# Performance work log

Measured on AMD Instinct MI355X. Metric: run time of the kernel, lower is better.

Reference implementation:

```python
import jax, jax.numpy as jnp
import numpy as np
from jax import lax

B, N, C = 16, 16384, 256          # batch, points, seed feature dim
P, NS = 256, 16                   # num_proposal, ball-query nsample
RADIUS = 0.3
NUM_CLASS, NUM_HEADING_BIN, NUM_SIZE = 18, 12, 18
OUT_FEAT = 2 + 3 + NUM_HEADING_BIN * 2 + NUM_SIZE * 4 + NUM_CLASS   # 119
PN2_NC = 128
MID_FEAT = (PN2_NC + OUT_FEAT) // 2                                 # 123
EPS = 1e-5

PARAM_NAMES = [f"mlp_{s}{i}" for i in range(3) for s in ("w", "b", "g", "be")] + [
    "c1_w", "c1_b", "bn1_g", "bn1_b", "c2_w", "c2_b", "bn2_g", "bn2_b", "c3_w", "c3_b"]


def setup_inputs():
    key = jax.random.key(0)
    ks = iter(jax.random.split(key, 32))
    def w(shape):
        return jax.random.normal(next(ks), shape, jnp.float32) / np.float32(np.sqrt(shape[0]))
    inp = {
        "pos":      jax.random.normal(next(ks), (B, N, 3), jnp.float32),
        "features": jax.random.normal(next(ks), (B, C, N), jnp.float32),
        "seed_pos": jax.random.normal(next(ks), (B, N, 3), jnp.float32),
    }
    dims = [3 + C, PN2_NC, PN2_NC, PN2_NC]
    for i in range(3):
        inp[f"mlp_w{i}"]  = w((dims[i], dims[i + 1]))
        inp[f"mlp_b{i}"]  = jnp.zeros((dims[i + 1],), jnp.float32)
        inp[f"mlp_g{i}"]  = jnp.ones((dims[i + 1],), jnp.float32)
        inp[f"mlp_be{i}"] = jnp.zeros((dims[i + 1],), jnp.float32)
    inp["c1_w"], inp["c1_b"] = w((PN2_NC, PN2_NC)), jnp.zeros((PN2_NC,), jnp.float32)
    inp["bn1_g"], inp["bn1_b"] = jnp.ones((PN2_NC,), jnp.float32), jnp.zeros((PN2_NC,), jnp.float32)
    inp["c2_w"], inp["c2_b"] = w((PN2_NC, MID_FEAT)), jnp.zeros((MID_FEAT,), jnp.float32)
    inp["bn2_g"], inp["bn2_b"] = jnp.ones((MID_FEAT,), jnp.float32), jnp.zeros((MID_FEAT,), jnp.float32)
    inp["c3_w"], inp["c3_b"] = w((MID_FEAT, OUT_FEAT)), jnp.zeros((OUT_FEAT,), jnp.float32)
    return inp


def _fps(p):
    # iterative furthest point sampling on one cloud p:[N,3] -> [P] int32 (starts at index 0)
    def step(carry, _):
        dists, far = carry
        d = jnp.sum((p - p[far]) ** 2, axis=-1)
        dists = jnp.minimum(dists, d)
        return (dists, jnp.argmax(dists).astype(jnp.int32)), far
    init = (jnp.full((p.shape[0],), 1e10, p.dtype), jnp.array(0, jnp.int32))
    _, idx = lax.scan(step, init, None, length=P)
    return idx


def _ball_query(new_pos, pos):
    # first NS points of pos within RADIUS of each center (CUDA ball_query semantics)
    d2 = jnp.sum((new_pos[:, :, None, :] - pos[:, None, :, :]) ** 2, -1)  # [B,P,N]
    n = pos.shape[1]
    ar = jnp.arange(n, dtype=jnp.int32)
    sortkey = jnp.where(d2 <= RADIUS ** 2, ar, ar + n)
    vals, idx = lax.top_k(-sortkey, NS)        # smallest keys = earliest in-radius indices
    valid = (-vals) < n
    return jnp.where(valid, idx, idx[..., :1])  # pad misses with first hit


def _bn(x, g, b, axes):
    m = jnp.mean(x, axes, keepdims=True)
    v = jnp.var(x, axes, keepdims=True)
    return (x - m) * lax.rsqrt(v + EPS) * g + b


def _forward(pos, features, seed_pos, params):
    idx_p = jax.vmap(_fps)(seed_pos)                              # seed_fps sampling [B,P]
    take = jax.vmap(lambda a, i: a[i])
    new_pos = take(pos, idx_p)                                    # [B,P,3]
    idx = _ball_query(new_pos, pos)                               # [B,P,NS]
    gp = take(pos, idx.reshape(B, -1)).reshape(B, P, NS, 3)
    gf = take(features.transpose(0, 2, 1), idx.reshape(B, -1)).reshape(B, P, NS, C)
    x = jnp.concatenate([gp - new_pos[:, :, None, :], gf], -1)    # [B,P,NS,3+C]
    for i in range(3):                                            # shared MLP (1x1 conv2d + BN + ReLU)
        x = jax.nn.relu(_bn(x @ params[f"mlp_w{i}"] + params[f"mlp_b{i}"],
                            params[f"mlp_g{i}"], params[f"mlp_be{i}"], (0, 1, 2)))
    x = jnp.max(x, axis=2)                                        # max over neighbors -> [B,P,128]
    x = jax.nn.relu(_bn(x @ params["c1_w"] + params["c1_b"], params["bn1_g"], params["bn1_b"], (0, 1)))
    x = jax.nn.relu(_bn(x @ params["c2_w"] + params["c2_b"], params["bn2_g"], params["bn2_b"], (0, 1)))
    x = x @ params["c3_w"] + params["c3_b"]                       # [B,P,OUT_FEAT]
    return x.transpose(0, 2, 1)                                   # [B,OUT_FEAT,P] like torch Conv1d


def reference(pos, features, seed_pos, mlp_w0, mlp_b0, mlp_g0, mlp_be0, mlp_w1, mlp_b1, mlp_g1, mlp_be1, mlp_w2, mlp_b2, mlp_g2, mlp_be2, c1_w, c1_b, bn1_g, bn1_b, c2_w, c2_b, bn2_g, bn2_b, c3_w, c3_b):
    ps = [mlp_w0, mlp_b0, mlp_g0, mlp_be0, mlp_w1, mlp_b1, mlp_g1, mlp_be1,
          mlp_w2, mlp_b2, mlp_g2, mlp_be2, c1_w, c1_b, bn1_g, bn1_b,
          c2_w, c2_b, bn2_g, bn2_b, c3_w, c3_b]
    params = dict(zip(PARAM_NAMES, ps))
    return _forward(pos, features, seed_pos, params)
```

## Files before the change

kernel.cpp:

```cpp
#include <hip/hip_runtime.h>

#define N_PTS 16384
#define BATCH 16
#define NPROP 256
#define NSAMP 16
#define CFEAT 256
#define KIN 259
#define KPAD 264
#define MBIG 65536
#define MSMALL 4096
#define NOUT 119
#define NBLK_BIG 512
#define NBLK_SMALL 64

#define FPS_LIST(M) M(0) M(1) M(2) M(3) M(4) M(5) M(6) M(7) \
  M(8) M(9) M(10) M(11) M(12) M(13) M(14) M(15) \
  M(16) M(17) M(18) M(19) M(20) M(21) M(22) M(23) \
  M(24) M(25) M(26) M(27) M(28) M(29) M(30) M(31)

#define FPS_PIN8(a,b,c,d,e,f,g,h) \
  asm volatile("" : "+v"(a), "+v"(b), "+v"(c), "+v"(d), \
                    "+v"(e), "+v"(f), "+v"(g), "+v"(h));

__global__ __attribute__((amdgpu_flat_work_group_size(512,512), amdgpu_waves_per_eu(2,2)))
void fps_kernel(const float* __restrict__ sp, const float* __restrict__ pos,
                int* __restrict__ idx_p, float* __restrict__ npos) {
#pragma clang fp contract(off)
  const int b = blockIdx.x;
  const int t = threadIdx.x;
  const int w = t >> 6;
  const int lane = t & 63;
  const float* base = sp + (size_t)b * N_PTS * 3;

#define FPS_DECL(J) float px##J, py##J, pz##J, dd##J;
  FPS_LIST(FPS_DECL)
#undef FPS_DECL

#define FPS_INIT(J) { const int i = t + J*512; \
    px##J = base[i*3+0]; py##J = base[i*3+1]; pz##J = base[i*3+2]; \
    dd##J = 1e10f; }
  FPS_LIST(FPS_INIT)
#undef FPS_INIT

  FPS_PIN8(px0,px1,px2,px3,px4,px5,px6,px7)
  FPS_PIN8(px8,px9,px10,px11,px12,px13,px14,px15)
  FPS_PIN8(px16,px17,px18,px19,px20,px21,px22,px23)
  FPS_PIN8(px24,px25,px26,px27,px28,px29,px30,px31)
  FPS_PIN8(py0,py1,py2,py3,py4,py5,py6,py7)
  FPS_PIN8(py8,py9,py10,py11,py12,py13,py14,py15)
  FPS_PIN8(py16,py17,py18,py19,py20,py21,py22,py23)
  FPS_PIN8(py24,py25,py26,py27,py28,py29,py30,py31)
  FPS_PIN8(pz0,pz1,pz2,pz3,pz4,pz5,pz6,pz7)
  FPS_PIN8(pz8,pz9,pz10,pz11,pz12,pz13,pz14,pz15)
  FPS_PIN8(pz16,pz17,pz18,pz19,pz20,pz21,pz22,pz23)
  FPS_PIN8(pz24,pz25,pz26,pz27,pz28,pz29,pz30,pz31)

  __shared__ unsigned long long part[2][8];
  __shared__ int sidx[NPROP];
  if (t == 0) { idx_p[b*NPROP] = 0; sidx[0] = 0; }
  float fx = base[0], fy = base[1], fz = base[2];
  for (int it = 1; it < NPROP; ++it) {
    float mv = -1.0f; int mi = 0;
#define FPS_STEP(J) { \
    float dx = px##J - fx, dy = py##J - fy, dz = pz##J - fz; \
    float d = (dx*dx + dy*dy) + dz*dz; \
    float nd = fminf(dd##J, d); \
    dd##J = nd; \
    if (nd > mv) { mv = nd; mi = t + J*512; } }
    FPS_LIST(FPS_STEP)
#undef FPS_STEP
    unsigned long long key =
      ((unsigned long long)__float_as_uint(mv) << 32) |
      (unsigned long long)(unsigned)(0x7FFFFFFF - mi);
#pragma unroll
    for (int o = 32; o > 0; o >>= 1) {
      unsigned long long ok = __shfl_xor(key, o, 64);
      if (ok > key) key = ok;
    }
    const int buf = it & 1;
    if (lane == 0) part[buf][w] = key;
    __syncthreads();
    unsigned long long k2 = part[buf][0];
#pragma unroll
    for (int q = 1; q < 8; ++q) {
      unsigned long long ok = part[buf][q];
      if (ok > k2) k2 = ok;
    }
    const int far = 0x7FFFFFFF - (int)(unsigned)(k2 & 0xFFFFFFFFull);
    if (t == 0) { idx_p[b*NPROP + it] = far; sidx[it] = far; }
    const float* fp = base + (size_t)far*3;
    fx = fp[0]; fy = fp[1]; fz = fp[2];
  }
  __syncthreads();
  if (t < NPROP) {
    const int ii = sidx[t];
    const float* pp = pos + ((size_t)b*N_PTS + ii)*3;
    float* np = npos + (size_t)(b*NPROP + t)*3;
    np[0] = pp[0]; np[1] = pp[1]; np[2] = pp[2];
  }
}

__global__ __launch_bounds__(256)
void ballq_kernel(const float* __restrict__ pos, const float* __restrict__ npos,
                  int* __restrict__ idxg) {
#pragma clang fp contract(off)
  __shared__ int res[4][NSAMP];
  const int tid = threadIdx.x;
  const int w = tid >> 6, lane = tid & 63;
  const int cid = blockIdx.x*4 + w;
  const int b = cid >> 8;
  const float R2 = (float)(0.3*0.3);
  if (lane == 0) res[w][0] = 0;
  const float cx = npos[cid*3+0], cy = npos[cid*3+1], cz = npos[cid*3+2];
  const float* pb = pos + (size_t)b*N_PTS*3;
  int cnt = 0;
  const unsigned long long lmask = (1ull << lane) - 1ull;
#pragma unroll 4
  for (int ch = 0; ch < N_PTS/64; ++ch) {
    int i = ch*64 + lane;
    float dx = pb[i*3+0]-cx, dy = pb[i*3+1]-cy, dz = pb[i*3+2]-cz;
    float d2 = (dx*dx + dy*dy) + dz*dz;
    bool pred = d2 <= R2;
    unsigned long long bal = __ballot(pred);
    if (pred) {
      int slot = cnt + (int)__popcll(bal & lmask);
      if (slot < NSAMP) res[w][slot] = i;
    }
    cnt += (int)__popcll(bal);
  }
  __syncthreads();
  if (lane < NSAMP) {
    int v = res[w][lane];
    if (lane >= cnt) v = res[w][0];
    idxg[cid*NSAMP + lane] = v;
  }
}

__global__ __launch_bounds__(256)
void prep_w(const float* __restrict__ w0, const float* __restrict__ c2w,
            const float* __restrict__ c2b, const float* __restrict__ c3w,
            const float* __restrict__ c3b,
            float* __restrict__ Wp0, float* __restrict__ Wp2, float* __restrict__ B2p,
            float* __restrict__ Wp3, float* __restrict__ B3p) {
  int g = blockIdx.x*256 + threadIdx.x;
  const int S0 = KPAD*128, S1 = S0 + 16384, S2 = S1 + 128, S3 = S2 + 16384, S4 = S3 + 128;
  if (g < S0) {
    int k = g >> 7, n = g & 127;
    Wp0[g] = (k < KIN) ? w0[k*128 + n] : 0.f;
  } else if (g < S1) {
    int g2 = g - S0; int k = g2 >> 7, n = g2 & 127;
    Wp2[g2] = (n < 123) ? c2w[k*123 + n] : 0.f;
  } else if (g < S2) {
    int n = g - S1;
    B2p[n] = (n < 123) ? c2b[n] : 0.f;
  } else if (g < S3) {
    int g2 = g - S2; int k = g2 >> 7, n = g2 & 127;
    Wp3[g2] = (k < 123 && n < NOUT) ? c3w[k*NOUT + n] : 0.f;
  } else if (g < S4) {
    int n = g - S3;
    B3p[n] = (n < NOUT) ? c3b[n] : 0.f;
  }
}

__global__ __launch_bounds__(256)
void gemm_l0(const float* __restrict__ pos, const float* __restrict__ npos,
             const float* __restrict__ feat, const int* __restrict__ idxg,
             const float* __restrict__ Wp, const float* __restrict__ bias,
             float* __restrict__ H, float* __restrict__ Sp, float* __restrict__ Qp) {
  __shared__ float As[8][128];
  __shared__ float Ws[8][128];
  __shared__ float pd[3][128];
  __shared__ int ids[128];
  const int tid = threadIdx.x;
  const int m0 = blockIdx.x * 128;
  const int b = m0 >> 12;
  const float* fb = feat + (size_t)b * CFEAT * N_PTS;
  if (tid < 128) {
    int m = m0 + tid;
    int ii = idxg[m];
    ids[tid] = ii;
    int q = m >> 4;
    const float* pp = pos + ((size_t)b*N_PTS + ii)*3;
    const float* cc = npos + (size_t)q*3;
    pd[0][tid] = pp[0] - cc[0];
    pd[1][tid] = pp[1] - cc[1];
    pd[2][tid] = pp[2] - cc[2];
  }
  __syncthreads();
  const int kr = tid >> 5;
  const int cm = (tid & 31) * 4;
  int ii_r[4];
#pragma unroll
  for (int x = 0; x < 4; ++x) ii_r[x] = ids[cm+x];
  float acc[8][8];
#pragma unroll
  for (int i = 0; i < 8; ++i)
#pragma unroll
    for (int j = 0; j < 8; ++j) acc[i][j] = 0.f;
  const int tm = tid & 15, tn = tid >> 4;
  for (int k0 = 0; k0 < KPAD; k0 += 8) {
    const int k = k0 + kr;
    float4 a0;
    if (k < 3) {
      a0.x = pd[k][cm+0]; a0.y = pd[k][cm+1]; a0.z = pd[k][cm+2]; a0.w = pd[k][cm+3];
    } else if (k < KIN) {
      const float* fr = fb + (size_t)(k-3)*N_PTS;
      a0.x = fr[ii_r[0]]; a0.y = fr[ii_r[1]]; a0.z = fr[ii_r[2]]; a0.w = fr[ii_r[3]];
    } else {
      a0 = make_float4(0.f,0.f,0.f,0.f);
    }
    float4 wv = *(const float4*)(Wp + (size_t)k*128 + cm);
    __syncthreads();
    *(float4*)&As[kr][cm] = a0;
    *(float4*)&Ws[kr][cm] = wv;
    __syncthreads();
#pragma unroll
    for (int kk = 0; kk < 8; ++kk) {
      float a[8], bb[8];
      *(float4*)(a)   = *(const float4*)&As[kk][tm*4];
      *(float4*)(a+4) = *(const float4*)&As[kk][tm*4 + 64];
      *(float4*)(bb)   = *(const float4*)&Ws[kk][tn*8];
      *(float4*)(bb+4) = *(const float4*)&Ws[kk][tn*8+4];
#pragma unroll
      for (int i = 0; i < 8; ++i)
#pragma unroll
        for (int j = 0; j < 8; ++j)
          acc[i][j] = fmaf(a[i], bb[j], acc[i][j]);
    }
  }
#pragma unroll
  for (int j = 0; j < 8; ++j) {
    const int n = tn*8 + j;
    const float bv = bias[n];
    float* cr = H + (size_t)n*MBIG + m0 + tm*4;
    float4 o0, o1;
    o0.x = acc[0][j]+bv; o0.y = acc[1][j]+bv; o0.z = acc[2][j]+bv; o0.w = acc[3][j]+bv;
    o1.x = acc[4][j]+bv; o1.y = acc[5][j]+bv; o1.z = acc[6][j]+bv; o1.w = acc[7][j]+bv;
    *(float4*)(cr)      = o0;
    *(float4*)(cr + 64) = o1;
    float s = o0.x+o0.y+o0.z+o0.w + o1.x+o1.y+o1.z+o1.w;
    float q = o0.x*o0.x+o0.y*o0.y+o0.z*o0.z+o0.w*o0.w
            + o1.x*o1.x+o1.y*o1.y+o1.z*o1.z+o1.w*o1.w;
#pragma unroll
    for (int o = 1; o < 16; o <<= 1) {
      s += __shfl_xor(s, o, 64);
      q += __shfl_xor(q, o, 64);
    }
    if (tm == 0) {
      Sp[(size_t)n*NBLK_BIG + blockIdx.x] = s;
      Qp[(size_t)n*NBLK_BIG + blockIdx.x] = q;
    }
  }
}

__global__ __launch_bounds__(256)
void gemm_big(const float* __restrict__ A, const float* __restrict__ W,
              const float* __restrict__ bias, const float* __restrict__ sc,
              const float* __restrict__ sh, float* __restrict__ C,
              float* __restrict__ Sp, float* __restrict__ Qp) {
  __shared__ float Ws[128][128];
  __shared__ float As[2][8][128];
  const int tid = threadIdx.x;
  const int m0 = blockIdx.x * 128;
  const int kr = tid >> 5;
  const int cw = (tid & 31) * 4;
  const int tm = tid & 15, tn = tid >> 4;
#pragma unroll
  for (int rr = 0; rr < 16; ++rr) {
    const int k = rr*8 + kr;
    *(float4*)&Ws[k][cw] = *(const float4*)(W + (size_t)k*128 + cw);
  }
  {
    float4 a0 = *(const float4*)(A + (size_t)kr*MBIG + m0 + cw);
    const float s_ = sc[kr], h_ = sh[kr];
    a0.x = fmaxf(fmaf(a0.x, s_, h_), 0.f);
    a0.y = fmaxf(fmaf(a0.y, s_, h_), 0.f);
    a0.z = fmaxf(fmaf(a0.z, s_, h_), 0.f);
    a0.w = fmaxf(fmaf(a0.w, s_, h_), 0.f);
    *(float4*)&As[0][kr][cw] = a0;
  }
  __syncthreads();
  float acc[8][8];
#pragma unroll
  for (int i = 0; i < 8; ++i)
#pragma unroll
    for (int j = 0; j < 8; ++j) acc[i][j] = 0.f;
  for (int step = 0; step < 16; ++step) {
    const int cur = step & 1;
    float4 a1;
    if (step < 15) {
      const int k = (step+1)*8 + kr;
      a1 = *(const float4*)(A + (size_t)k*MBIG + m0 + cw);
      const float s_ = sc[k], h_ = sh[k];
      a1.x = fmaxf(fmaf(a1.x, s_, h_), 0.f);
      a1.y = fmaxf(fmaf(a1.y, s_, h_), 0.f);
      a1.z = fmaxf(fmaf(a1.z, s_, h_), 0.f);
      a1.w = fmaxf(fmaf(a1.w, s_, h_), 0.f);
    }
#pragma unroll
    for (int kk = 0; kk < 8; ++kk) {
      float a[8], bb[8];
      *(float4*)(a)   = *(const float4*)&As[cur][kk][tm*4];
      *(float4*)(a+4) = *(const float4*)&As[cur][kk][tm*4 + 64];
      *(float4*)(bb)   = *(const float4*)&Ws[step*8+kk][tn*8];
      *(float4*)(bb+4) = *(const float4*)&Ws[step*8+kk][tn*8+4];
#pragma unroll
      for (int i = 0; i < 8; ++i)
#pragma unroll
        for (int j = 0; j < 8; ++j)
          acc[i][j] = fmaf(a[i], bb[j], acc[i][j]);
    }
    if (step < 15) *(float4*)&As[cur^1][kr][cw] = a1;
    __syncthreads();
  }
#pragma unroll
  for (int j = 0; j < 8; ++j) {
    const int n = tn*8 + j;
    const float bv = bias[n];
    float* cr = C + (size_t)n*MBIG + m0 + tm*4;
    float4 o0, o1;
    o0.x = acc[0][j]+bv; o0.y = acc[1][j]+bv; o0.z = acc[2][j]+bv; o0.w = acc[3][j]+bv;
    o1.x = acc[4][j]+bv; o1.y = acc[5][j]+bv; o1.z = acc[6][j]+bv; o1.w = acc[7][j]+bv;
    *(float4*)(cr)      = o0;
    *(float4*)(cr + 64) = o1;
    float s = o0.x+o0.y+o0.z+o0.w + o1.x+o1.y+o1.z+o1.w;
    float q = o0.x*o0.x+o0.y*o0.y+o0.z*o0.z+o0.w*o0.w
            + o1.x*o1.x+o1.y*o1.y+o1.z*o1.z+o1.w*o1.w;
#pragma unroll
    for (int o = 1; o < 16; o <<= 1) {
      s += __shfl_xor(s, o, 64);
      q += __shfl_xor(q, o, 64);
    }
    if (tm == 0) {
      Sp[(size_t)n*NBLK_BIG + blockIdx.x] = s;
      Qp[(size_t)n*NBLK_BIG + blockIdx.x] = q;
    }
  }
}

template<int TM, int MODE, int DOPART>
__global__ __launch_bounds__(256)
void gemm_k(const float* __restrict__ A, const float* __restrict__ W,
            const float* __restrict__ bias, const float* __restrict__ sc,
            const float* __restrict__ sh, float* __restrict__ C,
            float* __restrict__ Sp, float* __restrict__ Qp,
            int M, int K, int useT) {
  __shared__ float As[8][TM];
  __shared__ float Ws[8][128];
  const int tid = threadIdx.x;
  const int m0 = blockIdx.x * TM;
  const int kr = tid >> 5;
  const int cw = (tid & 31) * 4;
  const int tm = tid & 15, tn = tid >> 4;
  constexpr int MR = TM / 16;
  constexpr int NBLK = (TM == 128) ? NBLK_BIG : NBLK_SMALL;
  float acc[MR][8];
#pragma unroll
  for (int i = 0; i < MR; ++i)
#pragma unroll
    for (int j = 0; j < 8; ++j) acc[i][j] = 0.f;
  for (int k0 = 0; k0 < K; k0 += 8) {
    const float* ar = A + (size_t)(k0+kr)*M + m0;
    float4 wv = *(const float4*)(W + (size_t)(k0+kr)*128 + cw);
    const float s_ = useT ? sc[k0+kr] : 1.f;
    const float h_ = useT ? sh[k0+kr] : 0.f;
    const int c2 = (tid & 31) * 2;
    float2 a0 = *(const float2*)(ar + c2);
    if (useT) {
      a0.x = fmaxf(fmaf(a0.x, s_, h_), 0.f);
      a0.y = fmaxf(fmaf(a0.y, s_, h_), 0.f);
    }
    __syncthreads();
    *(float2*)&As[kr][c2] = a0;
    *(float4*)&Ws[kr][cw] = wv;
    __syncthreads();
#pragma unroll
    for (int kk = 0; kk < 8; ++kk) {
      float a[MR], bb[8];
      *(float4*)(a) = *(const float4*)&As[kk][tm*4];
      *(float4*)(bb)   = *(const float4*)&Ws[kk][tn*8];
      *(float4*)(bb+4) = *(const float4*)&Ws[kk][tn*8+4];
#pragma unroll
      for (int i = 0; i < MR; ++i)
#pragma unroll
        for (int j = 0; j < 8; ++j)
          acc[i][j] = fmaf(a[i], bb[j], acc[i][j]);
    }
  }
  if (MODE == 0) {
#pragma unroll
    for (int j = 0; j < 8; ++j) {
      const int n = tn*8 + j;
      const float bv = bias[n];
      float* cr = C + (size_t)n*M + m0 + tm*4;
      float4 o0;
      o0.x = acc[0][j]+bv; o0.y = acc[1][j]+bv; o0.z = acc[2][j]+bv; o0.w = acc[3][j]+bv;
      *(float4*)(cr) = o0;
      if constexpr (DOPART) {
        float s = o0.x+o0.y+o0.z+o0.w;
        float q = o0.x*o0.x+o0.y*o0.y+o0.z*o0.z+o0.w*o0.w;
#pragma unroll
        for (int o = 1; o < 16; o <<= 1) {
          s += __shfl_xor(s, o, 64);
          q += __shfl_xor(q, o, 64);
        }
        if (tm == 0) {
          Sp[(size_t)n*NBLK + blockIdx.x] = s;
          Qp[(size_t)n*NBLK + blockIdx.x] = q;
        }
      }
    }
  } else {
    const int bb_ = m0 >> 8;
    const int pcol = (m0 & 255) + tm*4;
#pragma unroll
    for (int j = 0; j < 8; ++j) {
      const int n = tn*8 + j;
      if (n < NOUT) {
        const float bv = bias[n];
        float* cr = C + ((size_t)bb_*NOUT + n)*256 + pcol;
        float4 o0;
        o0.x = acc[0][j]+bv; o0.y = acc[1][j]+bv; o0.z = acc[2][j]+bv; o0.w = acc[3][j]+bv;
        *(float4*)(cr) = o0;
      }
    }
  }
}

__global__ __launch_bounds__(256)
void stats_finish(const float* __restrict__ Sp, const float* __restrict__ Qp,
                  int nblk, int M, int nc,
                  const float* __restrict__ g, const float* __restrict__ be,
                  float* __restrict__ sc, float* __restrict__ sh) {
  const int c = blockIdx.x;
  const int tid = threadIdx.x;
  if (c >= nc) { if (tid == 0) { sc[c] = 0.f; sh[c] = 0.f; } return; }
  float s = 0.f, q = 0.f;
  for (int i = tid; i < nblk; i += 256) {
    s += Sp[(size_t)c*nblk + i];
    q += Qp[(size_t)c*nblk + i];
  }
#pragma unroll
  for (int o = 32; o > 0; o >>= 1) {
    s += __shfl_xor(s, o, 64);
    q += __shfl_xor(q, o, 64);
  }
  __shared__ float ws_[4], wq_[4];
  const int w = tid >> 6, lane = tid & 63;
  if (lane == 0) { ws_[w] = s; wq_[w] = q; }
  __syncthreads();
  if (tid == 0) {
    float S = ws_[0]+ws_[1]+ws_[2]+ws_[3];
    float Q = wq_[0]+wq_[1]+wq_[2]+wq_[3];
    float mean = S / (float)M;
    float var  = Q / (float)M - mean*mean;
    float inv  = rsqrtf(var + 1e-5f);
    float gg = g[c];
    sc[c] = inv * gg;
    sh[c] = be[c] - mean * inv * gg;
  }
}

__global__ __launch_bounds__(256)
void pool_kernel(const float* __restrict__ H2, const float* __restrict__ sc,
                 const float* __restrict__ sh, float* __restrict__ X3) {
  int gidx = blockIdx.x*256 + threadIdx.x;
  int c = gidx >> 12;
  int q = gidx & 4095;
  const float* src = H2 + (size_t)c*MBIG + (size_t)q*NSAMP;
  float s_ = sc[c], h_ = sh[c];
  float m = 0.f;
#pragma unroll
  for (int k = 0; k < NSAMP; k += 4) {
    float4 v = *(const float4*)(src + k);
    m = fmaxf(m, fmaf(v.x, s_, h_));
    m = fmaxf(m, fmaf(v.y, s_, h_));
    m = fmaxf(m, fmaf(v.z, s_, h_));
    m = fmaxf(m, fmaf(v.w, s_, h_));
  }
  X3[(size_t)c*MSMALL + q] = m;
}

extern "C" void kernel_launch(void* const* d_in, const int* in_sizes, int n_in,
                              void* d_out, int out_size, void* d_ws, size_t ws_size,
                              hipStream_t stream) {
  const float* pos  = (const float*)d_in[0];
  const float* feat = (const float*)d_in[1];
  const float* spos = (const float*)d_in[2];
  const float* w0  = (const float*)d_in[3];
  const float* b0  = (const float*)d_in[4];
  const float* g0  = (const float*)d_in[5];
  const float* be0 = (const float*)d_in[6];
  const float* w1  = (const float*)d_in[7];
  const float* b1  = (const float*)d_in[8];
  const float* g1  = (const float*)d_in[9];
  const float* be1 = (const float*)d_in[10];
  const float* w2  = (const float*)d_in[11];
  const float* b2  = (const float*)d_in[12];
  const float* g2  = (const float*)d_in[13];
  const float* be2 = (const float*)d_in[14];
  const float* c1w = (const float*)d_in[15];
  const float* c1b = (const float*)d_in[16];
  const float* bg1 = (const float*)d_in[17];
  const float* bb1 = (const float*)d_in[18];
  const float* c2w = (const float*)d_in[19];
  const float* c2b = (const float*)d_in[20];
  const float* bg2 = (const float*)d_in[21];
  const float* bb2 = (const float*)d_in[22];
  const float* c3w = (const float*)d_in[23];
  const float* c3b = (const float*)d_in[24];
  float* out = (float*)d_out;

  float* fws = (float*)d_ws;
  size_t off = 0;
  auto alloc = [&](size_t n) { float* p = fws + off; off += n; return p; };
  float* H0  = alloc((size_t)128*MBIG);
  float* H1  = alloc((size_t)128*MBIG);
  float* X3  = alloc((size_t)128*MSMALL);
  float* H3  = alloc((size_t)128*MSMALL);
  float* H4  = alloc((size_t)128*MSMALL);
  float* Wp0 = alloc(KPAD*128);
  float* Wp2 = alloc(16384);
  float* B2p = alloc(128);
  float* Wp3 = alloc(16384);
  float* B3p = alloc(128);
  float* sc0 = alloc(128); float* sh0 = alloc(128);
  float* sc1 = alloc(128); float* sh1 = alloc(128);
  float* sc2 = alloc(128); float* sh2 = alloc(128);
  float* sc3 = alloc(128); float* sh3 = alloc(128);
  float* sc4 = alloc(128); float* sh4 = alloc(128);
  float* Sp  = alloc((size_t)128*NBLK_BIG);
  float* Qp  = alloc((size_t)128*NBLK_BIG);
  float* npos = alloc((size_t)BATCH*NPROP*3);
  int* idx_p = (int*)alloc(BATCH*NPROP);
  int* idxg  = (int*)alloc(MBIG);
  float* H2 = H0;

  fps_kernel<<<BATCH, 512, 0, stream>>>(spos, pos, idx_p, npos);
  ballq_kernel<<<BATCH*NPROP/4, 256, 0, stream>>>(pos, npos, idxg);
  prep_w<<<261, 256, 0, stream>>>(w0, c2w, c2b, c3w, c3b, Wp0, Wp2, B2p, Wp3, B3p);

  gemm_l0<<<MBIG/128, 256, 0, stream>>>(pos, npos, feat, idxg, Wp0, b0, H0, Sp, Qp);
  stats_finish<<<128, 256, 0, stream>>>(Sp, Qp, NBLK_BIG, MBIG, 128, g0, be0, sc0, sh0);
  gemm_big<<<MBIG/128, 256, 0, stream>>>(H0, w1, b1, sc0, sh0, H1, Sp, Qp);
  stats_finish<<<128, 256, 0, stream>>>(Sp, Qp, NBLK_BIG, MBIG, 128, g1, be1, sc1, sh1);
  gemm_big<<<MBIG/128, 256, 0, stream>>>(H1, w2, b2, sc1, sh1, H2, Sp, Qp);
  stats_finish<<<128, 256, 0, stream>>>(Sp, Qp, NBLK_BIG, MBIG, 128, g2, be2, sc2, sh2);
  pool_kernel<<<128*MSMALL/256, 256, 0, stream>>>(H2, sc2, sh2, X3);

  gemm_k<64,0,1><<<MSMALL/64, 256, 0, stream>>>(X3, c1w, c1b, nullptr, nullptr, H3, Sp, Qp, MSMALL, 128, 0);
  stats_finish<<<128, 256, 0, stream>>>(Sp, Qp, NBLK_SMALL, MSMALL, 128, bg1, bb1, sc3, sh3);
  gemm_k<64,0,1><<<MSMALL/64, 256, 0, stream>>>(H3, Wp2, B2p, sc3, sh3, H4, Sp, Qp, MSMALL, 128, 1);
  stats_finish<<<128, 256, 0, stream>>>(Sp, Qp, NBLK_SMALL, MSMALL, 123, bg2, bb2, sc4, sh4);
  gemm_k<64,1,0><<<MSMALL/64, 256, 0, stream>>>(H4, Wp3, B3p, sc4, sh4, out, nullptr, nullptr, MSMALL, 128, 1);
}
```

Before: 855.8 us.

## Stage point tiles in LDS and process 16 ball-query centers per block

The ball-query kernel now loads 1024-point chunks of the cloud into shared memory with coalesced float4 reads, and each wave handles four query centers against the staged points. This reuses each point load across 16 centers instead of 4 and replaces strided global loads with LDS reads. Centers that already have 16 neighbors skip further distance checks in later chunks. The cost is extra block-wide barriers, and the grid shrinks to 256 blocks, which may reduce occupancy on the GPU.

```diff
diff --git a/kernel.cpp b/kernel.cpp
--- a/kernel.cpp
+++ b/kernel.cpp
@@ -104,35 +104,63 @@
 void ballq_kernel(const float* __restrict__ pos, const float* __restrict__ npos,
                   int* __restrict__ idxg) {
 #pragma clang fp contract(off)
-  __shared__ int res[4][NSAMP];
+  __shared__ float4 pts[1024];
+  __shared__ int res[16][NSAMP];
   const int tid = threadIdx.x;
   const int w = tid >> 6, lane = tid & 63;
-  const int cid = blockIdx.x*4 + w;
-  const int b = cid >> 8;
+  const int c0 = blockIdx.x * 16;
+  const int b = c0 >> 8;
   const float R2 = (float)(0.3*0.3);
-  if (lane == 0) res[w][0] = 0;
-  const float cx = npos[cid*3+0], cy = npos[cid*3+1], cz = npos[cid*3+2];
-  const float* pb = pos + (size_t)b*N_PTS*3;
-  int cnt = 0;
+  if (tid < 16) res[tid][0] = 0;
+  float cx[4], cy[4], cz[4];
+  int cnt[4];
+#pragma unroll
+  for (int j = 0; j < 4; ++j) {
+    const int cid = c0 + w*4 + j;
+    cx[j] = npos[cid*3+0]; cy[j] = npos[cid*3+1]; cz[j] = npos[cid*3+2];
+    cnt[j] = 0;
+  }
+  const float4* pb4 = (const float4*)(pos + (size_t)b*N_PTS*3);
   const unsigned long long lmask = (1ull << lane) - 1ull;
-#pragma unroll 4
-  for (int ch = 0; ch < N_PTS/64; ++ch) {
-    int i = ch*64 + lane;
-    float dx = pb[i*3+0]-cx, dy = pb[i*3+1]-cy, dz = pb[i*3+2]-cz;
-    float d2 = (dx*dx + dy*dy) + dz*dz;
-    bool pred = d2 <= R2;
-    unsigned long long bal = __ballot(pred);
-    if (pred) {
-      int slot = cnt + (int)__popcll(bal & lmask);
-      if (slot < NSAMP) res[w][slot] = i;
-    }
-    cnt += (int)__popcll(bal);
+  for (int ch = 0; ch < 16; ++ch) {
+    float4 A = pb4[ch*768 + tid*3 + 0];
+    float4 B = pb4[ch*768 + tid*3 + 1];
+    float4 C = pb4[ch*768 + tid*3 + 2];
+    __syncthreads();
+    pts[tid*4+0] = make_float4(A.x, A.y, A.z, 0.f);
+    pts[tid*4+1] = make_float4(A.w, B.x, B.y, 0.f);
+    pts[tid*4+2] = make_float4(B.z, B.w, C.x, 0.f);
+    pts[tid*4+3] = make_float4(C.y, C.z, C.w, 0.f);
+    __syncthreads();
+#pragma unroll
+    for (int j = 0; j < 4; ++j) {
+      if (cnt[j] < NSAMP) {
+        int cj = cnt[j];
+        for (int g = 0; g < 16; ++g) {
+          const float4 v = pts[g*64 + lane];
+          float dx = v.x - cx[j], dy = v.y - cy[j], dz = v.z - cz[j];
+          float d2 = (dx*dx + dy*dy) + dz*dz;
+          bool pred = d2 <= R2;
+          unsigned long long bal = __ballot(pred);
+          if (pred) {
+            int slot = cj + (int)__popcll(bal & lmask);
+            if (slot < NSAMP) res[w*4+j][slot] = ch*1024 + g*64 + lane;
+          }
+          cj += (int)__popcll(bal);
+        }
+        cnt[j] = cj;
+      }
+    }
   }
   __syncthreads();
   if (lane < NSAMP) {
-    int v = res[w][lane];
-    if (lane >= cnt) v = res[w][0];
-    idxg[cid*NSAMP + lane] = v;
+#pragma unroll
+    for (int j = 0; j < 4; ++j) {
+      const int cid = c0 + w*4 + j;
+      int v = res[w*4+j][lane];
+      if (lane >= cnt[j]) v = res[w*4+j][0];
+      idxg[cid*NSAMP + lane] = v;
+    }
   }
 }
 
@@ -537,7 +565,7 @@
   float* H2 = H0;
 
   fps_kernel<<<BATCH, 512, 0, stream>>>(spos, pos, idx_p, npos);
-  ballq_kernel<<<BATCH*NPROP/4, 256, 0, stream>>>(pos, npos, idxg);
+  ballq_kernel<<<BATCH*NPROP/16, 256, 0, stream>>>(pos, npos, idxg);
   prep_w<<<261, 256, 0, stream>>>(w0, c2w, c2b, c3w, c3b, Wp0, Wp2, B2p, Wp3, B3p);
 
   gemm_l0<<<MBIG/128, 256, 0, stream>>>(pos, npos, feat, idxg, Wp0, b0, H0, Sp, Qp);
```

New measurement: 827.9 us. 1.03x faster.
